# Performance work log

Hardware: AMD Instinct MI355X
Metric: run time of the kernel (lower is better)

## Reference

```python
import jax, jax.numpy as jnp
import numpy as np

KH = KW = 3
STRIDE = 1
PAD = 1
DIL = 1

def setup_inputs() -> dict:
    key = jax.random.key(0)
    k1, k2, k3, k4, k5 = jax.random.split(key, 5)
    B, C, H, W = 8, 256, 64, 64
    O = 256
    inp = jax.random.normal(k1, (B, C, H, W), dtype=jnp.float32)
    offset = jax.random.normal(k2, (B, 2 * KH * KW, H, W), dtype=jnp.float32)
    mask = jax.random.uniform(k3, (B, KH * KW, H, W), dtype=jnp.float32)
    weight = jax.random.normal(k4, (O, C, KH, KW), dtype=jnp.float32) * (1.0 / np.sqrt(C * KH * KW))
    bias = jax.random.normal(k5, (O,), dtype=jnp.float32) * 0.01
    return {"input": inp, "offset": offset, "mask": mask, "weight": weight, "bias": bias}


def _gather(img_flat, idx):
    # img_flat: [C, H*W], idx: [K2, Ho, Wo] -> [C, K2, Ho, Wo]
    return img_flat[:, idx]


def _deform_conv2d(inp, offset, mask, weight, bias):
    B, C, H, W = inp.shape
    O = weight.shape[0]
    K2 = KH * KW
    Ho = (H + 2 * PAD - DIL * (KH - 1) - 1) // STRIDE + 1
    Wo = (W + 2 * PAD - DIL * (KW - 1) - 1) // STRIDE + 1

    # offset layout: channel 2*k is dy, 2*k+1 is dx for kernel tap k
    off = offset.reshape(B, K2, 2, Ho, Wo)
    off_y, off_x = off[:, :, 0], off[:, :, 1]  # [B, K2, Ho, Wo]

    ki = (jnp.arange(K2) // KW) * DIL  # kernel row offset per tap
    kj = (jnp.arange(K2) % KW) * DIL   # kernel col offset per tap
    base_y = (jnp.arange(Ho) * STRIDE - PAD)[None, :, None] + ki[:, None, None]  # [K2,Ho,1]
    base_x = (jnp.arange(Wo) * STRIDE - PAD)[None, None, :] + kj[:, None, None]  # [K2,1,Wo]

    y = off_y + base_y[None]  # [B, K2, Ho, Wo]
    x = off_x + base_x[None]

    y0 = jnp.floor(y)
    x0 = jnp.floor(x)
    ly = y - y0
    lx = x - x0
    hy = 1.0 - ly
    hx = 1.0 - lx
    y0i = y0.astype(jnp.int32)
    x0i = x0.astype(jnp.int32)

    img_flat = inp.reshape(B, C, H * W)

    def corner(yy, xx, w):
        valid = (yy >= 0) & (yy < H) & (xx >= 0) & (xx < W)
        idx = jnp.clip(yy, 0, H - 1) * W + jnp.clip(xx, 0, W - 1)  # [B,K2,Ho,Wo]
        vals = jax.vmap(_gather)(img_flat, idx)  # [B,C,K2,Ho,Wo]
        wgt = jnp.where(valid, w, 0.0)[:, None]  # [B,1,K2,Ho,Wo]
        return vals * wgt

    sampled = (corner(y0i, x0i, hy * hx)
               + corner(y0i, x0i + 1, hy * lx)
               + corner(y0i + 1, x0i, ly * hx)
               + corner(y0i + 1, x0i + 1, ly * lx))  # [B,C,K2,Ho,Wo]

    sampled = sampled * mask[:, None]  # modulated deformable conv v2

    w2 = weight.reshape(O, C, K2)
    out = jnp.einsum('bckhw,ock->bohw', sampled, w2) + bias[None, :, None, None]
    return out


def reference(input, offset, mask, weight, bias):
    return _deform_conv2d(input, offset, mask, weight, bias)
```

## Files before the change

### kernel.cpp

```cpp
#include <hip/hip_runtime.h>

typedef _Float16 f16x8 __attribute__((ext_vector_type(8)));
typedef float    f32x4 __attribute__((ext_vector_type(4)));

namespace {
constexpr int Bb = 8, Cc = 256, Oo = 256;
constexpr int HW = 4096;
constexpr int NCH2 = 36;
constexpr int SROW2 = 72;
constexpr int TBLK = 512;
}

__device__ inline f16x8 sp8(_Float16 x) { f16x8 r = {x,x,x,x,x,x,x,x}; return r; }

__device__ __forceinline__ void barrier_lgkm() {
  asm volatile("s_waitcnt lgkmcnt(0)" ::: "memory");
  __builtin_amdgcn_s_barrier();
}

__global__ __launch_bounds__(256)
void prep(const float* __restrict__ in, const float* __restrict__ w,
          _Float16* __restrict__ outh, _Float16* __restrict__ wh) {
  const int bid = blockIdx.x;
  const int t   = threadIdx.x;
  if (bid < TBLK) {
    __shared__ _Float16 Lt[64][264];
    const int b = bid >> 6, pxg = bid & 63;
    const float* src = in + (size_t)b * Cc * HW + pxg * 64;
    const int chb = t & 15, quad = t >> 4;
#pragma unroll
    for (int ci = 0; ci < 16; ++ci) {
      int ch = ci * 16 + chb;
      float4 v = *(const float4*)(src + (size_t)ch * HW + quad * 4);
      Lt[quad * 4 + 0][ch] = (_Float16)v.x;
      Lt[quad * 4 + 1][ch] = (_Float16)v.y;
      Lt[quad * 4 + 2][ch] = (_Float16)v.z;
      Lt[quad * 4 + 3][ch] = (_Float16)v.w;
    }
    __syncthreads();
    _Float16* dst = outh + ((size_t)b * HW + pxg * 64) * Cc;
    const int c8 = t & 31, pxs = t >> 5;
#pragma unroll
    for (int it = 0; it < 8; ++it) {
      int px = it * 8 + pxs;
      f16x8 v = *(const f16x8*)(&Lt[px][c8 * 8]);
      *(f16x8*)(dst + (size_t)px * Cc + c8 * 8) = v;
    }
  } else {
    int tt = (bid - TBLK) * 256 + t;
    int o  = tt & 255;
    int Kb = (tt >> 8) * 8;
    const float* s = w + (size_t)o * 2304;
    f16x8 v;
#pragma unroll
    for (int k8 = 0; k8 < 8; ++k8) {
      int K = Kb + k8;
      int tap = K >> 8, c = K & 255;
      v[k8] = (_Float16)s[c * 9 + tap];
    }
    *(f16x8*)(wh + (size_t)tt * 8) = v;
  }
}

__global__ __launch_bounds__(512, 2)
void dcn_mfma(const _Float16* __restrict__ inh,
              const _Float16* __restrict__ wgh,
              const float* __restrict__ offset,
              const float* __restrict__ mask,
              const float* __restrict__ bias,
              float* __restrict__ out) {
  __shared__ __align__(16) _Float16 Sl[2][128 * SROW2];

  const int tid = threadIdx.x;
  const int b   = blockIdx.x;
  const int rp  = blockIdx.y;

  const int pos = tid >> 2, cg = tid & 3;
  const int ho  = rp * 2 + (pos >> 6), wo = pos & 63;
  const int lane = tid & 63, wm = tid >> 6;
  const int lq = lane >> 4, lr = lane & 15;

  const f16x8* gin = (const f16x8*)(inh + (size_t)b * HW * Cc);
  const uint4* wg4 = (const uint4*)wgh;
  const int    wbase = lq * 256 + wm * 32 + lr;

  int4   mi_c, mi_n = {0,0,0,0};
  float4 mwt_c, mwt_n = {0,0,0,0};
  float  ofy, ofx, msk;
  f16x8  vc[2][8];
  uint4  awv[4];

  auto load_md_inputs = [&](int tap) {
    ofy = offset[(((size_t)b * 18 + 2 * tap)     * 64 + ho) * 64 + wo];
    ofx = offset[(((size_t)b * 18 + 2 * tap + 1) * 64 + ho) * 64 + wo];
    msk = mask  [(((size_t)b * 9  + tap)         * 64 + ho) * 64 + wo];
  };
  auto build_md = [&](int tap, int4& mio, float4& mwo) {
    int ki = tap / 3, kj = tap % 3;
    float y = ofy + (float)(ho - 1 + ki);
    float x = ofx + (float)(wo - 1 + kj);
    float y0f = floorf(y), x0f = floorf(x);
    float ly = y - y0f, lx = x - x0f;
    float hy = 1.f - ly, hx = 1.f - lx;
    int y0 = (int)y0f, x0 = (int)x0f;
    int y1 = y0 + 1, x1 = x0 + 1;
    bool vy0 = (unsigned)y0 < 64u, vy1 = (unsigned)y1 < 64u;
    bool vx0 = (unsigned)x0 < 64u, vx1 = (unsigned)x1 < 64u;
    int cy0 = min(max(y0, 0), 63), cy1 = min(max(y1, 0), 63);
    int cx0 = min(max(x0, 0), 63), cx1 = min(max(x1, 0), 63);
    mwo.x = (vy0 && vx0) ? hy * hx * msk : 0.f;
    mwo.y = (vy0 && vx1) ? hy * lx * msk : 0.f;
    mwo.z = (vy1 && vx0) ? ly * hx * msk : 0.f;
    mwo.w = (vy1 && vx1) ? ly * lx * msk : 0.f;
    mio = make_int4(cy0 * 64 + cx0, cy0 * 64 + cx1, cy1 * 64 + cx0, cy1 * 64 + cx1);
  };
  auto gather = [&](const int4& m, int cc, f16x8* dst) {
    int cb = (cc & 3) * 8 + cg;
    dst[0] = gin[m.x * 32 + cb];     dst[1] = gin[m.y * 32 + cb];
    dst[2] = gin[m.z * 32 + cb];     dst[3] = gin[m.w * 32 + cb];
    dst[4] = gin[m.x * 32 + cb + 4]; dst[5] = gin[m.y * 32 + cb + 4];
    dst[6] = gin[m.z * 32 + cb + 4]; dst[7] = gin[m.w * 32 + cb + 4];
  };
  auto stage = [&](const f16x8* v, const float4& w, int buf) {
    f16x8 s0 = v[0] * sp8((_Float16)w.x) + v[1] * sp8((_Float16)w.y)
             + v[2] * sp8((_Float16)w.z) + v[3] * sp8((_Float16)w.w);
    f16x8 s1 = v[4] * sp8((_Float16)w.x) + v[5] * sp8((_Float16)w.y)
             + v[6] * sp8((_Float16)w.z) + v[7] * sp8((_Float16)w.w);
    *(f16x8*)(&Sl[buf][pos * SROW2 + cg * 8])      = s0;
    *(f16x8*)(&Sl[buf][pos * SROW2 + 32 + cg * 8]) = s1;
  };
  auto wload_half = [&](int cc, int h) {
    const uint4* base = wg4 + (size_t)(2 * cc + h) * 1024 + wbase;
#pragma unroll
    for (int mt = 0; mt < 2; ++mt) awv[h * 2 + mt] = base[mt * 16];
  };

  f32x4 acc[2][8];
#pragma unroll
  for (int mt = 0; mt < 2; ++mt)
#pragma unroll
    for (int nt = 0; nt < 8; ++nt) {
      acc[mt][nt][0] = 0.f; acc[mt][nt][1] = 0.f;
      acc[mt][nt][2] = 0.f; acc[mt][nt][3] = 0.f;
    }

  load_md_inputs(0);
  build_md(0, mi_c, mwt_c);
  gather(mi_c, 0, vc[0]);
  wload_half(0, 0); wload_half(0, 1);
  gather(mi_c, 1, vc[1]);
  stage(vc[0], mwt_c, 0);
  barrier_lgkm();

  for (int t = 0; t < 9; ++t) {
#pragma unroll
    for (int j = 0; j < 4; ++j) {
      const int cc  = t * 4 + j;
      const int cur = j & 1;

      if (j < 2) {
        gather(mi_c, cc + 2, vc[cur]);
      } else if (t < 8) {
        if (j == 2) build_md(t + 1, mi_n, mwt_n);
        gather(mi_n, cc + 2, vc[cur]);
      }
      if (j == 0 && t < 8) load_md_inputs(t + 1);

      {
        f16x8 afr[2];
#pragma unroll
        for (int mt = 0; mt < 2; ++mt) afr[mt] = __builtin_bit_cast(f16x8, awv[mt]);
        if (cc + 1 < NCH2) wload_half(cc + 1, 0);
#pragma unroll
        for (int nt = 0; nt < 8; ++nt) {
          f16x8 bfr = *(const f16x8*)(&Sl[cur][(nt * 16 + lr) * SROW2 + lq * 8]);
#pragma unroll
          for (int mt = 0; mt < 2; ++mt)
            acc[mt][nt] = __builtin_amdgcn_mfma_f32_16x16x32_f16(afr[mt], bfr, acc[mt][nt], 0, 0, 0);
        }
      }
      {
        f16x8 afr[2];
#pragma unroll
        for (int mt = 0; mt < 2; ++mt) afr[mt] = __builtin_bit_cast(f16x8, awv[2 + mt]);
        if (cc + 1 < NCH2) wload_half(cc + 1, 1);
#pragma unroll
        for (int nt = 0; nt < 8; ++nt) {
          f16x8 bfr = *(const f16x8*)(&Sl[cur][(nt * 16 + lr) * SROW2 + 32 + lq * 8]);
#pragma unroll
          for (int mt = 0; mt < 2; ++mt)
            acc[mt][nt] = __builtin_amdgcn_mfma_f32_16x16x32_f16(afr[mt], bfr, acc[mt][nt], 0, 0, 0);
        }
      }

      if (j < 3) {
        stage(vc[cur ^ 1], mwt_c, cur ^ 1);
      } else if (t < 8) {
        stage(vc[cur ^ 1], mwt_n, cur ^ 1);
      }
      barrier_lgkm();
    }
    if (t < 8) { mi_c = mi_n; mwt_c = mwt_n; }
  }

#pragma unroll
  for (int mt = 0; mt < 2; ++mt) {
#pragma unroll
    for (int reg = 0; reg < 4; ++reg) {
      int o = wm * 32 + mt * 16 + lq * 4 + reg;
      float bv = bias[o];
      float* op = out + ((size_t)(b * 256 + o)) * 4096 + rp * 128 + lr;
#pragma unroll
      for (int nt = 0; nt < 8; ++nt)
        op[nt * 16] = acc[mt][nt][reg] + bv;
    }
  }
}

extern "C" void kernel_launch(void* const* d_in, const int* in_sizes, int n_in,
                              void* d_out, int out_size, void* d_ws, size_t ws_size,
                              hipStream_t stream) {
  const float* inp    = (const float*)d_in[0];
  const float* offset = (const float*)d_in[1];
  const float* mask   = (const float*)d_in[2];
  const float* weight = (const float*)d_in[3];
  const float* bias   = (const float*)d_in[4];
  float* out = (float*)d_out;

  _Float16* inh = (_Float16*)d_ws;
  _Float16* wgh = inh + (size_t)Bb * HW * Cc;

  hipLaunchKernelGGL(prep, dim3(TBLK + 288), dim3(256), 0, stream,
                     inp, weight, inh, wgh);
  hipLaunchKernelGGL(dcn_mfma, dim3(Bb, 32), dim3(512), 0, stream,
                     inh, wgh, offset, mask, bias, out);
}
```

Baseline: 141.2 us.

## Double block size to 16 waves, each computing 16 output channels

```diff
diff --git a/kernel.cpp b/kernel.cpp
--- a/kernel.cpp
+++ b/kernel.cpp
@@ -62,7 +62,7 @@
   }
 }
 
-__global__ __launch_bounds__(512, 2)
+__global__ __launch_bounds__(1024, 4)
 void dcn_mfma(const _Float16* __restrict__ inh,
               const _Float16* __restrict__ wgh,
               const float* __restrict__ offset,
@@ -75,20 +75,20 @@
   const int b   = blockIdx.x;
   const int rp  = blockIdx.y;
 
-  const int pos = tid >> 2, cg = tid & 3;
+  const int pos = tid >> 3, cg = tid & 7;
   const int ho  = rp * 2 + (pos >> 6), wo = pos & 63;
   const int lane = tid & 63, wm = tid >> 6;
   const int lq = lane >> 4, lr = lane & 15;
 
   const f16x8* gin = (const f16x8*)(inh + (size_t)b * HW * Cc);
   const uint4* wg4 = (const uint4*)wgh;
-  const int    wbase = lq * 256 + wm * 32 + lr;
+  const int    wbase = lq * 256 + wm * 16 + lr;
 
   int4   mi_c, mi_n = {0,0,0,0};
   float4 mwt_c, mwt_n = {0,0,0,0};
   float  ofy, ofx, msk;
-  f16x8  vc[2][8];
-  uint4  awv[4];
+  f16x8  vc[2][4];
+  uint4  awv[2];
 
   auto load_md_inputs = [&](int tap) {
     ofy = offset[(((size_t)b * 18 + 2 * tap)     * 64 + ho) * 64 + wo];
@@ -116,33 +116,23 @@
   };
   auto gather = [&](const int4& m, int cc, f16x8* dst) {
     int cb = (cc & 3) * 8 + cg;
-    dst[0] = gin[m.x * 32 + cb];     dst[1] = gin[m.y * 32 + cb];
-    dst[2] = gin[m.z * 32 + cb];     dst[3] = gin[m.w * 32 + cb];
-    dst[4] = gin[m.x * 32 + cb + 4]; dst[5] = gin[m.y * 32 + cb + 4];
-    dst[6] = gin[m.z * 32 + cb + 4]; dst[7] = gin[m.w * 32 + cb + 4];
+    dst[0] = gin[m.x * 32 + cb];  dst[1] = gin[m.y * 32 + cb];
+    dst[2] = gin[m.z * 32 + cb];  dst[3] = gin[m.w * 32 + cb];
   };
   auto stage = [&](const f16x8* v, const float4& w, int buf) {
     f16x8 s0 = v[0] * sp8((_Float16)w.x) + v[1] * sp8((_Float16)w.y)
              + v[2] * sp8((_Float16)w.z) + v[3] * sp8((_Float16)w.w);
-    f16x8 s1 = v[4] * sp8((_Float16)w.x) + v[5] * sp8((_Float16)w.y)
-             + v[6] * sp8((_Float16)w.z) + v[7] * sp8((_Float16)w.w);
-    *(f16x8*)(&Sl[buf][pos * SROW2 + cg * 8])      = s0;
-    *(f16x8*)(&Sl[buf][pos * SROW2 + 32 + cg * 8]) = s1;
+    *(f16x8*)(&Sl[buf][pos * SROW2 + cg * 8]) = s0;
   };
   auto wload_half = [&](int cc, int h) {
-    const uint4* base = wg4 + (size_t)(2 * cc + h) * 1024 + wbase;
-#pragma unroll
-    for (int mt = 0; mt < 2; ++mt) awv[h * 2 + mt] = base[mt * 16];
-  };
-
-  f32x4 acc[2][8];
-#pragma unroll
-  for (int mt = 0; mt < 2; ++mt)
-#pragma unroll
-    for (int nt = 0; nt < 8; ++nt) {
-      acc[mt][nt][0] = 0.f; acc[mt][nt][1] = 0.f;
-      acc[mt][nt][2] = 0.f; acc[mt][nt][3] = 0.f;
-    }
+    awv[h] = wg4[(size_t)(2 * cc + h) * 1024 + wbase];
+  };
+
+  f32x4 acc[8];
+#pragma unroll
+  for (int nt = 0; nt < 8; ++nt) {
+    acc[nt][0] = 0.f; acc[nt][1] = 0.f; acc[nt][2] = 0.f; acc[nt][3] = 0.f;
+  }
 
   load_md_inputs(0);
   build_md(0, mi_c, mwt_c);
@@ -167,29 +157,21 @@
       if (j == 0 && t < 8) load_md_inputs(t + 1);
 
       {
-        f16x8 afr[2];
-#pragma unroll
-        for (int mt = 0; mt < 2; ++mt) afr[mt] = __builtin_bit_cast(f16x8, awv[mt]);
+        f16x8 afr = __builtin_bit_cast(f16x8, awv[0]);
         if (cc + 1 < NCH2) wload_half(cc + 1, 0);
 #pragma unroll
         for (int nt = 0; nt < 8; ++nt) {
           f16x8 bfr = *(const f16x8*)(&Sl[cur][(nt * 16 + lr) * SROW2 + lq * 8]);
-#pragma unroll
-          for (int mt = 0; mt < 2; ++mt)
-            acc[mt][nt] = __builtin_amdgcn_mfma_f32_16x16x32_f16(afr[mt], bfr, acc[mt][nt], 0, 0, 0);
+          acc[nt] = __builtin_amdgcn_mfma_f32_16x16x32_f16(afr, bfr, acc[nt], 0, 0, 0);
         }
       }
       {
-        f16x8 afr[2];
-#pragma unroll
-        for (int mt = 0; mt < 2; ++mt) afr[mt] = __builtin_bit_cast(f16x8, awv[2 + mt]);
+        f16x8 afr = __builtin_bit_cast(f16x8, awv[1]);
         if (cc + 1 < NCH2) wload_half(cc + 1, 1);
 #pragma unroll
         for (int nt = 0; nt < 8; ++nt) {
           f16x8 bfr = *(const f16x8*)(&Sl[cur][(nt * 16 + lr) * SROW2 + 32 + lq * 8]);
-#pragma unroll
-          for (int mt = 0; mt < 2; ++mt)
-            acc[mt][nt] = __builtin_amdgcn_mfma_f32_16x16x32_f16(afr[mt], bfr, acc[mt][nt], 0, 0, 0);
+          acc[nt] = __builtin_amdgcn_mfma_f32_16x16x32_f16(afr, bfr, acc[nt], 0, 0, 0);
         }
       }
 
@@ -204,16 +186,13 @@
   }
 
 #pragma unroll
-  for (int mt = 0; mt < 2; ++mt) {
-#pragma unroll
-    for (int reg = 0; reg < 4; ++reg) {
-      int o = wm * 32 + mt * 16 + lq * 4 + reg;
-      float bv = bias[o];
-      float* op = out + ((size_t)(b * 256 + o)) * 4096 + rp * 128 + lr;
-#pragma unroll
-      for (int nt = 0; nt < 8; ++nt)
-        op[nt * 16] = acc[mt][nt][reg] + bv;
-    }
+  for (int reg = 0; reg < 4; ++reg) {
+    int o = wm * 16 + lq * 4 + reg;
+    float bv = bias[o];
+    float* op = out + ((size_t)(b * 256 + o)) * 4096 + rp * 128 + lr;
+#pragma unroll
+    for (int nt = 0; nt < 8; ++nt)
+      op[nt * 16] = acc[nt][reg] + bv;
   }
 }
 
@@ -232,6 +211,6 @@
 
   hipLaunchKernelGGL(prep, dim3(TBLK + 288), dim3(256), 0, stream,
                      inp, weight, inh, wgh);
-  hipLaunchKernelGGL(dcn_mfma, dim3(Bb, 32), dim3(512), 0, stream,
+  hipLaunchKernelGGL(dcn_mfma, dim3(Bb, 32), dim3(1024), 0, stream,
                      inh, wgh, offset, mask, bias, out);
 }
```

New measurement: 153.0 us. 8.3% more time.
